# Optimization experiments

Hardware: AMD Instinct MI355X
Metric: run time of the kernel (lower is better)

## Reference

```python
import jax, jax.numpy as jnp
import numpy as np

N_NODES = 50000
N_EDGES = 600000
N_COMM = 500
COMM_EDGES = 8000
NFEAT = 128
NHID = 128
NCLASS = 10
NLAYERS = 3
NHEADS = 8
EPS = 1e-5


def setup_inputs() -> dict:
    key = jax.random.key(0)
    ks = jax.random.split(key, 32)
    s = 0.05
    def rn(i, shape, scale=s):
        return (jax.random.normal(ks[i], shape, dtype=jnp.float32) * scale)
    return {
        "node_features": jax.random.normal(ks[0], (N_NODES, NFEAT), dtype=jnp.float32),
        "node_edge_index": jax.random.randint(ks[1], (2, N_EDGES), 0, N_NODES),
        "comm_features": jax.random.normal(ks[2], (N_COMM, NHID), dtype=jnp.float32),
        "comm_edge_index": jax.random.randint(ks[3], (2, COMM_EDGES), 0, N_COMM),
        "node_to_comm_map": jax.random.randint(ks[4], (N_NODES,), 0, N_COMM),
        # node-branch GCN params (nfeat == nhid so weights stack)
        "node_W": rn(5, (NLAYERS, NHID, NHID)),
        "node_b": rn(6, (NLAYERS, NHID)),
        "node_bn_g": 1.0 + rn(7, (NLAYERS, NHID)),
        "node_bn_b": rn(8, (NLAYERS, NHID)),
        # community-branch GCN params
        "comm_W": rn(9, (NLAYERS, NHID, NHID)),
        "comm_b": rn(10, (NLAYERS, NHID)),
        "comm_bn_g": 1.0 + rn(11, (NLAYERS, NHID)),
        "comm_bn_b": rn(12, (NLAYERS, NHID)),
        # MultiheadAttention params (torch layout: y = x @ W.T + b)
        "attn_in_w": rn(13, (3 * NHID, NHID)),
        "attn_in_b": rn(14, (3 * NHID,)),
        "attn_out_w": rn(15, (NHID, NHID)),
        "attn_out_b": rn(16, (NHID,)),
        # gate LayerNorm
        "ln_g": 1.0 + rn(17, (NHID,)),
        "ln_b": rn(18, (NHID,)),
        # classifier: Linear(128,64) -> BN -> ReLU -> Linear(64,10)
        "cls_W1": rn(19, (NHID, NHID // 2)),
        "cls_b1": rn(20, (NHID // 2,)),
        "cls_bn_g": 1.0 + rn(21, (NHID // 2,)),
        "cls_bn_b": rn(22, (NHID // 2,)),
        "cls_W2": rn(23, (NHID // 2, NCLASS)),
        "cls_b2": rn(24, (NCLASS,)),
    }


def _gcn_norm(edge_index, n):
    # PyG gcn_norm: add self-loops, symmetric D^-1/2 (A+I) D^-1/2
    loop = jnp.arange(n)
    src = jnp.concatenate([edge_index[0], loop])
    dst = jnp.concatenate([edge_index[1], loop])
    deg = jax.ops.segment_sum(jnp.ones(src.shape[0], jnp.float32), dst, num_segments=n)
    dinv = jnp.where(deg > 0, deg ** -0.5, 0.0)
    return src, dst, dinv[src] * dinv[dst]


def _gcn_stack(x, edge_index, Ws, bs, gs, betas):
    n = x.shape[0]
    src, dst, norm = _gcn_norm(edge_index, n)
    h = x
    for i in range(Ws.shape[0]):
        h_prev = h
        m = h @ Ws[i]  # linear commutes with normalized aggregation
        agg = jax.ops.segment_sum(m[src] * norm[:, None], dst, num_segments=n) + bs[i]
        mu = agg.mean(0)
        var = agg.var(0)  # biased, as torch BN training
        hb = (agg - mu) / jnp.sqrt(var + EPS) * gs[i] + betas[i]
        h = jax.nn.relu(hb)
        if i > 0:
            h = h + h_prev
    return h


def _mha(x, wi, bi, wo, bo):
    # x: [N, S=2, E]
    N, S, E = x.shape
    dh = E // NHEADS
    qkv = x @ wi.T + bi
    q, k, v = jnp.split(qkv, 3, axis=-1)
    q = q.reshape(N, S, NHEADS, dh)
    k = k.reshape(N, S, NHEADS, dh)
    v = v.reshape(N, S, NHEADS, dh)
    att = jnp.einsum('nqhd,nkhd->nhqk', q, k) / np.float32(np.sqrt(dh))
    att = jax.nn.softmax(att, axis=-1)
    o = jnp.einsum('nhqk,nkhd->nqhd', att, v).reshape(N, S, E)
    return o @ wo.T + bo


def reference(node_features, node_edge_index, comm_features, comm_edge_index,
              node_to_comm_map, node_W, node_b, node_bn_g, node_bn_b,
              comm_W, comm_b, comm_bn_g, comm_bn_b,
              attn_in_w, attn_in_b, attn_out_w, attn_out_b,
              ln_g, ln_b, cls_W1, cls_b1, cls_bn_g, cls_bn_b, cls_W2, cls_b2):
    h_node = _gcn_stack(node_features, node_edge_index, node_W, node_b, node_bn_g, node_bn_b)
    h_comm = _gcn_stack(comm_features, comm_edge_index, comm_W, comm_b, comm_bn_g, comm_bn_b)
    safe = jnp.clip(node_to_comm_map, 0, h_comm.shape[0] - 1)
    h_comm_exp = h_comm[safe]  # [N, nhid] cross-scale gather
    comb = jnp.stack([h_node, h_comm_exp], axis=1)  # [N, 2, nhid]
    attended = _mha(comb, attn_in_w, attn_in_b, attn_out_w, attn_out_b)
    x = attended.mean(axis=1) + h_node
    mu = x.mean(-1, keepdims=True)
    var = x.var(-1, keepdims=True)
    h_final = (x - mu) / jnp.sqrt(var + EPS) * ln_g + ln_b
    z = h_final @ cls_W1 + cls_b1
    zm = z.mean(0)
    zv = z.var(0)
    z = jax.nn.relu((z - zm) / jnp.sqrt(zv + EPS) * cls_bn_g + cls_bn_b)
    logits = z @ cls_W2 + cls_b2
    return jax.nn.log_softmax(logits, axis=-1)
```

## Files before the change

kernel.cpp:

```cpp
#include <hip/hip_runtime.h>
#include <hip/hip_bf16.h>
#include <cstdint>
#include <cstddef>


typedef __attribute__((ext_vector_type(8))) short bf16x8;
typedef __attribute__((ext_vector_type(4))) float f32x4;

#define EPSV 1e-5f

__device__ __forceinline__ float b2f(unsigned short u) {
    union { unsigned int i; float f; } x; x.i = ((unsigned int)u) << 16; return x.f;
}
__device__ __forceinline__ unsigned short f2b(float f) {
    union { float f; unsigned int i; } x; x.f = f;
    unsigned int i = x.i;
    return (unsigned short)((i + 0x7fffu + ((i >> 16) & 1u)) >> 16);
}

__global__ void prep_kernel(const float* __restrict__ node_W, const float* __restrict__ comm_W,
                            const float* __restrict__ cls_W1, const float* __restrict__ attn_in_w,
                            const float* __restrict__ attn_out_w, const float* __restrict__ comm_feat,
                            const float* __restrict__ node_feat,
                            unsigned short* __restrict__ WtN, unsigned short* __restrict__ WtC,
                            unsigned short* __restrict__ W1t, unsigned short* __restrict__ WinB,
                            unsigned short* __restrict__ WoutB, unsigned short* __restrict__ cfb,
                            unsigned short* __restrict__ nfb, int nC128, int nN128) {
    int idx = blockIdx.x * 256 + threadIdx.x;
    if (idx < 49152) {
        int l = idx >> 14, e = idx & 16383;
        int j = e & 7, lane = (e >> 3) & 63, kc = (e >> 9) & 3, t = e >> 11;
        int col = t * 16 + (lane & 15);
        int k = (lane >> 4) * 8 + kc * 32 + j;
        WtN[idx] = f2b(node_W[l * 16384 + k * 128 + col]); return;
    }
    idx -= 49152;
    if (idx < 49152) {
        int l = idx >> 14, e = idx & 16383;
        int j = e & 7, lane = (e >> 3) & 63, kc = (e >> 9) & 3, t = e >> 11;
        int col = t * 16 + (lane & 15);
        int k = (lane >> 4) * 8 + kc * 32 + j;
        WtC[idx] = f2b(comm_W[l * 16384 + k * 128 + col]); return;
    }
    idx -= 49152;
    if (idx < 8192) {
        int e = idx;
        int j = e & 7, lane = (e >> 3) & 63, kc = (e >> 9) & 3, t = e >> 11;
        int col = t * 16 + (lane & 15);
        int k = (lane >> 4) * 8 + kc * 32 + j;
        W1t[idx] = f2b(cls_W1[k * 64 + col]); return;
    }
    idx -= 8192;
    if (idx < 49152) {
        int e = idx;
        int j = e & 7, lane = (e >> 3) & 63, kc = (e >> 9) & 3, t = e >> 11;
        int col = t * 16 + (lane & 15);
        int k = (lane >> 4) * 8 + kc * 32 + j;
        WinB[idx] = f2b(attn_in_w[col * 128 + k]); return;
    }
    idx -= 49152;
    if (idx < 16384) {
        int e = idx;
        int j = e & 7, lane = (e >> 3) & 63, kc = (e >> 9) & 3, t = e >> 11;
        int col = t * 16 + (lane & 15);
        int k = (lane >> 4) * 8 + kc * 32 + j;
        WoutB[idx] = f2b(attn_out_w[col * 128 + k]); return;
    }
    idx -= 16384;
    if (idx < nC128) { cfb[idx] = f2b(comm_feat[idx]); return; }
    idx -= nC128;
    if (idx < nN128) { nfb[idx] = f2b(node_feat[idx]); }
}

__global__ void count_dual(const int* __restrict__ nd, int* __restrict__ cnt_n, int nE,
                           const int* __restrict__ cd, int* __restrict__ cnt_c, int cE) {
    int t = blockIdx.x * 256 + threadIdx.x;
    if (t < nE) atomicAdd(&cnt_n[nd[t]], 1);
    else if (t - nE < cE) atomicAdd(&cnt_c[cd[t - nE]], 1);
}

__global__ void dinv_dual(const int* __restrict__ cnt_n, float* __restrict__ di_n, int nN,
                          const int* __restrict__ cnt_c, float* __restrict__ di_c, int nC) {
    int t = blockIdx.x * 256 + threadIdx.x;
    if (t < nN) di_n[t] = rsqrtf((float)cnt_n[t] + 1.0f);
    else if (t - nN < nC) di_c[t - nN] = rsqrtf((float)cnt_c[t - nN] + 1.0f);
}

__global__ void scan_block_dual(const int* __restrict__ cnt_n, int* __restrict__ rs_n,
                                int* __restrict__ bsum_n, int nN, int nbN,
                                const int* __restrict__ cnt_c, int* __restrict__ rs_c,
                                int* __restrict__ bsum_c, int nC) {
    __shared__ int tmp[2048];
    const int* cnt; int* excl; int* bsum; int n, lb;
    if ((int)blockIdx.x < nbN) { cnt = cnt_n; excl = rs_n; bsum = bsum_n; n = nN; lb = blockIdx.x; }
    else { cnt = cnt_c; excl = rs_c; bsum = bsum_c; n = nC; lb = blockIdx.x - nbN; }
    int tid = threadIdx.x;
    int gid = lb * 1024 + tid;
    int v = (gid < n) ? ((cnt[gid] + 7) & ~7) : 0;
    int buf = 0;
    tmp[tid] = v;
    __syncthreads();
    for (int d = 1; d < 1024; d <<= 1) {
        int t = tmp[buf * 1024 + tid];
        int add = (tid >= d) ? tmp[buf * 1024 + tid - d] : 0;
        tmp[(1 - buf) * 1024 + tid] = t + add;
        buf = 1 - buf;
        __syncthreads();
    }
    int inc = tmp[buf * 1024 + tid];
    if (gid < n) excl[gid] = inc - v;
    if (tid == 1023) bsum[lb] = inc;
}

__global__ void scan_sums_dual(int* __restrict__ bsum_n, int nbN,
                               int* __restrict__ bsum_c, int nbC) {
    if (threadIdx.x == 0) {
        int acc = 0;
        for (int i = 0; i < nbN; ++i) { int t = bsum_n[i]; bsum_n[i] = acc; acc += t; }
    } else if (threadIdx.x == 1) {
        int acc = 0;
        for (int i = 0; i < nbC; ++i) { int t = bsum_c[i]; bsum_c[i] = acc; acc += t; }
    }
}

__global__ void scan_add_dual(int* __restrict__ rs_n, const int* __restrict__ bsum_n, int nN,
                              int* __restrict__ rs_c, const int* __restrict__ bsum_c, int nC) {
    int gid = blockIdx.x * 256 + threadIdx.x;
    if (gid < nN) rs_n[gid] += bsum_n[gid >> 10];
    else {
        int g = gid - nN;
        if (g < nC) rs_c[g] += bsum_c[g >> 10];
    }
}

__global__ void fill_dual(const int* __restrict__ ns, const int* __restrict__ ndst,
                          const float* __restrict__ di_n, const int* __restrict__ rs_n,
                          int* __restrict__ cur_n, int* __restrict__ csrc_n,
                          float* __restrict__ cw_n, int nE,
                          const int* __restrict__ cs, const int* __restrict__ cdst,
                          const float* __restrict__ di_c, const int* __restrict__ rs_c,
                          int* __restrict__ cur_c, int* __restrict__ csrc_c,
                          float* __restrict__ cw_c, int cE) {
    int e = blockIdx.x * 256 + threadIdx.x;
    if (e < nE) {
        int s = ns[e], d = ndst[e];
        int pos = atomicAdd(&cur_n[d], 1);
        int slot = rs_n[d] + pos;
        csrc_n[slot] = s;
        cw_n[slot] = di_n[s] * di_n[d];
    } else if (e - nE < cE) {
        int ee = e - nE;
        int s = cs[ee], d = cdst[ee];
        int pos = atomicAdd(&cur_c[d], 1);
        int slot = rs_c[d] + pos;
        csrc_c[slot] = s;
        cw_c[slot] = di_c[s] * di_c[d];
    }
}

__device__ __forceinline__ void gemm_wave_128(const unsigned short* __restrict__ A,
                                              const unsigned short* __restrict__ Bt,
                                              unsigned short* __restrict__ D,
                                              int M, int m0, int lane) {
    int r = lane & 15, q = lane >> 4;
    int arow = m0 + r; if (arow >= M) arow = M - 1;
    const unsigned short* ap = A + (size_t)arow * 128 + q * 8;
    bf16x8 afrag[4];
#pragma unroll
    for (int kc = 0; kc < 4; ++kc)
        afrag[kc] = *(const bf16x8*)(const void*)(ap + kc * 32);
#pragma unroll
    for (int tt = 0; tt < 8; ++tt) {
        f32x4 acc = {0.f, 0.f, 0.f, 0.f};
#pragma unroll
        for (int kc = 0; kc < 4; ++kc) {
            bf16x8 bfrag = *(const bf16x8*)(const void*)(Bt + (((size_t)tt * 4 + kc) << 9) + lane * 8);
            acc = __builtin_amdgcn_mfma_f32_16x16x32_bf16(afrag[kc], bfrag, acc, 0, 0, 0);
        }
        int n0 = tt * 16;
#pragma unroll
        for (int t = 0; t < 4; ++t) {
            int row = m0 + q * 4 + t;
            if (row < M) D[(size_t)row * 128 + n0 + r] = f2b(acc[t]);
        }
    }
}

__global__ __launch_bounds__(256) void gemm_dual(
    const unsigned short* __restrict__ A0, const unsigned short* __restrict__ Bt0,
    unsigned short* __restrict__ D0, int M0, int blocksA,
    const unsigned short* __restrict__ A1, const unsigned short* __restrict__ Bt1,
    unsigned short* __restrict__ D1, int M1) {
    int blk = blockIdx.x;
    const unsigned short *A, *Bt; unsigned short* D; int M, lb;
    if (blk < blocksA) { A = A0; Bt = Bt0; D = D0; M = M0; lb = blk; }
    else { A = A1; Bt = Bt1; D = D1; M = M1; lb = blk - blocksA; }
    int m0 = (lb * 4 + (int)(threadIdx.x >> 6)) * 16;
    if (m0 >= M) return;
    gemm_wave_128(A, Bt, D, M, m0, threadIdx.x & 63);
}

__global__ void gemm_kernel(const unsigned short* __restrict__ A,
                            const unsigned short* __restrict__ Bt,
                            const float* __restrict__ bias,
                            float* __restrict__ D, int M, int Ncol) {
    int wave = (blockIdx.x * blockDim.x + threadIdx.x) >> 6;
    int lane = threadIdx.x & 63;
    int m0 = wave * 16;
    if (m0 >= M) return;
    int r = lane & 15, q = lane >> 4;
    int arow = m0 + r; if (arow >= M) arow = M - 1;
    const unsigned short* ap = A + (size_t)arow * 128 + q * 8;
    bf16x8 afrag[4];
#pragma unroll
    for (int kc = 0; kc < 4; ++kc)
        afrag[kc] = *(const bf16x8*)(const void*)(ap + kc * 32);
    int ntiles = Ncol >> 4;
    for (int tt = 0; tt < ntiles; ++tt) {
        f32x4 acc = {0.f, 0.f, 0.f, 0.f};
#pragma unroll
        for (int kc = 0; kc < 4; ++kc) {
            bf16x8 bfrag = *(const bf16x8*)(const void*)(Bt + (((size_t)tt * 4 + kc) << 9) + lane * 8);
            acc = __builtin_amdgcn_mfma_f32_16x16x32_bf16(afrag[kc], bfrag, acc, 0, 0, 0);
        }
        int n0 = tt * 16;
        float bv = bias[n0 + r];
#pragma unroll
        for (int t = 0; t < 4; ++t) {
            int row = m0 + q * 4 + t;
            if (row < M) D[(size_t)row * Ncol + n0 + r] = acc[t] + bv;
        }
    }
}

__global__ __launch_bounds__(256) void gather_dual(
    const unsigned short* __restrict__ m0, const int* __restrict__ rs0,
    const int* __restrict__ cnt0,
    const int* __restrict__ cs0, const float* __restrict__ cw0,
    const float* __restrict__ di0, const float* __restrict__ b0,
    float* __restrict__ agg0, int n0, int blocksA,
    const unsigned short* __restrict__ m1, const int* __restrict__ rs1,
    const int* __restrict__ cnt1,
    const int* __restrict__ cs1, const float* __restrict__ cw1,
    const float* __restrict__ di1, const float* __restrict__ b1,
    float* __restrict__ agg1, int n1) {
    int blk = blockIdx.x;
    const unsigned short* m; const int *rs, *cnt, *cs; const float *cw, *di, *bias;
    float *agg; int n, lb;
    if (blk < blocksA) { m = m0; rs = rs0; cnt = cnt0; cs = cs0; cw = cw0; di = di0; bias = b0; agg = agg0; n = n0; lb = blk; }
    else { m = m1; rs = rs1; cnt = cnt1; cs = cs1; cw = cw1; di = di1; bias = b1; agg = agg1; n = n1; lb = blk - blocksA; }
    int wib = threadIdx.x >> 6, lane = threadIdx.x & 63;
    int node = lb * 4 + wib;
    if (node >= n) return;
    int start = rs[node];
    int end = start + ((cnt[node] + 7) & ~7);
    float a0 = 0.f, a1 = 0.f;
    for (int i = start; i < end; i += 8) {
        int   s[8]; float w[8]; unsigned int v[8];
#pragma unroll
        for (int j = 0; j < 8; ++j) { s[j] = cs[i + j]; w[j] = cw[i + j]; }
#pragma unroll
        for (int j = 0; j < 8; ++j)
            v[j] = *(const unsigned int*)(m + (size_t)s[j] * 128 + 2 * lane);
#pragma unroll
        for (int j = 0; j < 8; ++j) {
            a0 += b2f((unsigned short)(v[j] & 0xffff)) * w[j];
            a1 += b2f((unsigned short)(v[j] >> 16)) * w[j];
        }
    }
    float d = di[node]; float wself = d * d;
    unsigned int v = *(const unsigned int*)(m + (size_t)node * 128 + 2 * lane);
    a0 += b2f((unsigned short)(v & 0xffff)) * wself + bias[2 * lane];
    a1 += b2f((unsigned short)(v >> 16)) * wself + bias[2 * lane + 1];
    float2 o; o.x = a0; o.y = a1;
    ((float2*)(agg + (size_t)node * 128))[lane] = o;
}

__global__ __launch_bounds__(256) void stats_dual(
    const float* __restrict__ agg0, float* __restrict__ sums0, int n0, int blocksA,
    const float* __restrict__ agg1, float* __restrict__ sums1, int n1) {
    __shared__ float rsum[256], rsq[256];
    int blk = blockIdx.x;
    const float* agg; float* sums; int n, lb, nb;
    if (blk < blocksA) { agg = agg0; sums = sums0; n = n0; lb = blk; nb = blocksA; }
    else { agg = agg1; sums = sums1; n = n1; lb = blk - blocksA; nb = gridDim.x - blocksA; }
    int rpb = (n + nb - 1) / nb;
    int t = threadIdx.x;
    int f = t & 127, half = t >> 7;
    int r0 = lb * rpb, r1 = r0 + rpb; if (r1 > n) r1 = n;
    float s = 0.f, s2 = 0.f;
    for (int r = r0 + half; r < r1; r += 2) {
        float v = agg[(size_t)r * 128 + f];
        s += v; s2 += v * v;
    }
    rsum[t] = s; rsq[t] = s2;
    __syncthreads();
    if (t < 128) atomicAdd(&sums[t], rsum[t] + rsum[t + 128]);
    else atomicAdd(&sums[128 + f], rsq[f] + rsq[t]);
}

__global__ __launch_bounds__(256) void apply_dual(
    const float* __restrict__ agg0, const float* __restrict__ sums0,
    const float* __restrict__ g0, const float* __restrict__ be0,
    unsigned short* __restrict__ hb0, int n0, int blocksA, int useRes,
    const float* __restrict__ agg1, const float* __restrict__ sums1,
    const float* __restrict__ g1, const float* __restrict__ be1,
    unsigned short* __restrict__ hb1, int n1) {
    __shared__ float sc[128], sh[128];
    int blk = blockIdx.x;
    const float *agg, *sums, *g, *be; unsigned short* hb; int n, lb;
    if (blk < blocksA) { agg = agg0; sums = sums0; g = g0; be = be0; hb = hb0; n = n0; lb = blk; }
    else { agg = agg1; sums = sums1; g = g1; be = be1; hb = hb1; n = n1; lb = blk - blocksA; }
    int t = threadIdx.x;
    if (t < 128) {
        float inv = 1.f / (float)n;
        float mean = sums[t] * inv;
        float var = sums[128 + t] * inv - mean * mean;
        float rstd = rsqrtf(var + EPSV);
        float s = g[t] * rstd;
        sc[t] = s;
        sh[t] = be[t] - mean * s;
    }
    __syncthreads();
    int base = lb * 1024 + t * 4;
    if (base < n * 128) {
        float4 a = *(const float4*)(agg + base);
        ushort4 h = *(const ushort4*)(hb + base);
        int f = base & 127;
        float v0 = fmaxf(a.x * sc[f] + sh[f], 0.f);
        float v1 = fmaxf(a.y * sc[f + 1] + sh[f + 1], 0.f);
        float v2 = fmaxf(a.z * sc[f + 2] + sh[f + 2], 0.f);
        float v3 = fmaxf(a.w * sc[f + 3] + sh[f + 3], 0.f);
        if (useRes) { v0 += b2f(h.x); v1 += b2f(h.y); v2 += b2f(h.z); v3 += b2f(h.w); }
        ushort4 o; o.x = f2b(v0); o.y = f2b(v1); o.z = f2b(v2); o.w = f2b(v3);
        *(ushort4*)(hb + base) = o;
    }
}

__global__ __launch_bounds__(256) void mha_fused_kernel(
    const unsigned short* __restrict__ hbn, const unsigned short* __restrict__ hbc,
    const int* __restrict__ map,
    const unsigned short* __restrict__ WinB, const float* __restrict__ bin,
    const unsigned short* __restrict__ WoutB, const float* __restrict__ bout,
    const float* __restrict__ lng, const float* __restrict__ lnb,
    unsigned short* __restrict__ hfin, int nN, int nC) {
    __shared__ unsigned short obf_s[16 * 144];
    __shared__ float att_s[8 * 132];

    int b = blockIdx.x;
    int hg = threadIdx.x >> 6;
    int lane = threadIdx.x & 63;
    int r = lane & 15, q = lane >> 4;

    int anode = b * 8 + (r >> 1);
    if (anode >= nN) anode = nN - 1;
    const unsigned short* arow;
    if (r & 1) {
        int c = map[anode]; c = c < 0 ? 0 : (c >= nC ? nC - 1 : c);
        arow = hbc + (size_t)c * 128;
    } else {
        arow = hbn + (size_t)anode * 128;
    }
    bf16x8 afrag[4];
#pragma unroll
    for (int kc = 0; kc < 4; ++kc)
        afrag[kc] = *(const bf16x8*)(const void*)(arow + q * 8 + kc * 32);

    f32x4 qa[2], ka[2], va[2];
#pragma unroll
    for (int p = 0; p < 3; ++p) {
#pragma unroll
        for (int c = 0; c < 2; ++c) {
            int tt = p * 8 + hg * 2 + c;
            f32x4 acc = {0.f, 0.f, 0.f, 0.f};
#pragma unroll
            for (int kc = 0; kc < 4; ++kc) {
                bf16x8 bfrag = *(const bf16x8*)(const void*)(WinB + (((size_t)tt * 4 + kc) << 9) + lane * 8);
                acc = __builtin_amdgcn_mfma_f32_16x16x32_bf16(afrag[kc], bfrag, acc, 0, 0, 0);
            }
            float bv = bin[tt * 16 + r];
#pragma unroll
            for (int t = 0; t < 4; ++t) acc[t] += bv;
            if (p == 0) qa[c] = acc; else if (p == 1) ka[c] = acc; else va[c] = acc;
        }
    }

#pragma unroll
    for (int c = 0; c < 2; ++c) {
        float s00 = qa[c][0] * ka[c][0], s01 = qa[c][0] * ka[c][1];
        float s10 = qa[c][1] * ka[c][0], s11 = qa[c][1] * ka[c][1];
        float u00 = qa[c][2] * ka[c][2], u01 = qa[c][2] * ka[c][3];
        float u10 = qa[c][3] * ka[c][2], u11 = qa[c][3] * ka[c][3];
#pragma unroll
        for (int mku = 1; mku <= 8; mku <<= 1) {
            s00 += __shfl_xor(s00, mku); s01 += __shfl_xor(s01, mku);
            s10 += __shfl_xor(s10, mku); s11 += __shfl_xor(s11, mku);
            u00 += __shfl_xor(u00, mku); u01 += __shfl_xor(u01, mku);
            u10 += __shfl_xor(u10, mku); u11 += __shfl_xor(u11, mku);
        }
        s00 *= 0.25f; s01 *= 0.25f; s10 *= 0.25f; s11 *= 0.25f;
        u00 *= 0.25f; u01 *= 0.25f; u10 *= 0.25f; u11 *= 0.25f;
        float m0 = fmaxf(s00, s01), m1 = fmaxf(s10, s11);
        float m2 = fmaxf(u00, u01), m3 = fmaxf(u10, u11);
        float e00 = __expf(s00 - m0), e01 = __expf(s01 - m0);
        float e10 = __expf(s10 - m1), e11 = __expf(s11 - m1);
        float f00 = __expf(u00 - m2), f01 = __expf(u01 - m2);
        float f10 = __expf(u10 - m3), f11 = __expf(u11 - m3);
        float i0 = 1.f / (e00 + e01), i1 = 1.f / (e10 + e11);
        float i2 = 1.f / (f00 + f01), i3 = 1.f / (f10 + f11);
        float o0 = (e00 * va[c][0] + e01 * va[c][1]) * i0;
        float o1 = (e10 * va[c][0] + e11 * va[c][1]) * i1;
        float o2 = (f00 * va[c][2] + f01 * va[c][3]) * i2;
        float o3 = (f10 * va[c][2] + f11 * va[c][3]) * i3;
        int ocol = (hg * 2 + c) * 16 + r;
        obf_s[(q * 4 + 0) * 144 + ocol] = f2b(o0);
        obf_s[(q * 4 + 1) * 144 + ocol] = f2b(o1);
        obf_s[(q * 4 + 2) * 144 + ocol] = f2b(o2);
        obf_s[(q * 4 + 3) * 144 + ocol] = f2b(o3);
    }
    __syncthreads();

    bf16x8 ofrag[4];
#pragma unroll
    for (int kc = 0; kc < 4; ++kc)
        ofrag[kc] = *(const bf16x8*)(const void*)(obf_s + r * 144 + q * 8 + kc * 32);
#pragma unroll
    for (int c = 0; c < 2; ++c) {
        int tt = hg * 2 + c;
        f32x4 acc = {0.f, 0.f, 0.f, 0.f};
#pragma unroll
        for (int kc = 0; kc < 4; ++kc) {
            bf16x8 bfrag = *(const bf16x8*)(const void*)(WoutB + (((size_t)tt * 4 + kc) << 9) + lane * 8);
            acc = __builtin_amdgcn_mfma_f32_16x16x32_bf16(ofrag[kc], bfrag, acc, 0, 0, 0);
        }
        int n0 = tt * 16;
        float bv = bout[n0 + r];
        att_s[(q * 2 + 0) * 132 + n0 + r] = 0.5f * (acc[0] + acc[1]) + bv;
        att_s[(q * 2 + 1) * 132 + n0 + r] = 0.5f * (acc[2] + acc[3]) + bv;
    }
    __syncthreads();

    {
        int nl = threadIdx.x >> 5;
        int j2 = threadIdx.x & 31;
        int gnode = b * 8 + nl; if (gnode >= nN) gnode = nN - 1;
        const unsigned short* hrow = hbn + (size_t)gnode * 128 + j2 * 4;
        float x[4]; float s = 0.f, s2 = 0.f;
#pragma unroll
        for (int i = 0; i < 4; ++i) {
            x[i] = att_s[nl * 132 + j2 * 4 + i] + b2f(hrow[i]);
            s += x[i]; s2 += x[i] * x[i];
        }
        s += __shfl_xor(s, 1);  s2 += __shfl_xor(s2, 1);
        s += __shfl_xor(s, 2);  s2 += __shfl_xor(s2, 2);
        s += __shfl_xor(s, 4);  s2 += __shfl_xor(s2, 4);
        s += __shfl_xor(s, 8);  s2 += __shfl_xor(s2, 8);
        s += __shfl_xor(s, 16); s2 += __shfl_xor(s2, 16);
        float mu = s * (1.f / 128.f);
        float var = s2 * (1.f / 128.f) - mu * mu;
        float rstd = rsqrtf(var + EPSV);
        ushort4 o;
        o.x = f2b((x[0] - mu) * rstd * lng[j2 * 4]     + lnb[j2 * 4]);
        o.y = f2b((x[1] - mu) * rstd * lng[j2 * 4 + 1] + lnb[j2 * 4 + 1]);
        o.z = f2b((x[2] - mu) * rstd * lng[j2 * 4 + 2] + lnb[j2 * 4 + 2]);
        o.w = f2b((x[3] - mu) * rstd * lng[j2 * 4 + 3] + lnb[j2 * 4 + 3]);
        *(ushort4*)(hfin + (size_t)gnode * 128 + j2 * 4) = o;
    }
}

__global__ __launch_bounds__(256) void stats64_kernel(const float* __restrict__ z,
                                                      float* __restrict__ sums, int N) {
    __shared__ float ls[4][64], lsq[4][64];
    int f = threadIdx.x & 63, rg = threadIdx.x >> 6;
    int r0 = blockIdx.x * 64 + rg * 16;
    int r1 = r0 + 16; if (r1 > N) r1 = N;
    float s = 0.f, s2 = 0.f;
    for (int r = r0; r < r1; ++r) {
        float v = z[(size_t)r * 64 + f];
        s += v; s2 += v * v;
    }
    ls[rg][f] = s; lsq[rg][f] = s2;
    __syncthreads();
    int t = threadIdx.x;
    if (t < 64) atomicAdd(&sums[t], ls[0][t] + ls[1][t] + ls[2][t] + ls[3][t]);
    else if (t < 128) { int c = t - 64; atomicAdd(&sums[64 + c], lsq[0][c] + lsq[1][c] + lsq[2][c] + lsq[3][c]); }
}

__global__ __launch_bounds__(256) void final_kernel(const float* __restrict__ z,
                                                    const float* __restrict__ sums,
                                                    const float* __restrict__ g,
                                                    const float* __restrict__ be,
                                                    const float* __restrict__ W2,
                                                    const float* __restrict__ b2v,
                                                    float* __restrict__ out, int nN) {
    int node = blockIdx.x * 4 + (threadIdx.x >> 6);
    int lane = threadIdx.x & 63;
    float inv = 1.f / (float)nN;
    float mean = sums[lane] * inv;
    float var = sums[64 + lane] * inv - mean * mean;
    float sc = g[lane] * rsqrtf(var + EPSV);
    float sh = be[lane] - mean * sc;
    float v = 0.f;
    if (node < nN) v = fmaxf(z[(size_t)node * 64 + lane] * sc + sh, 0.f);
    float p[10];
    const float* wrow = W2 + lane * 10;
#pragma unroll
    for (int c = 0; c < 10; ++c) p[c] = v * wrow[c];
#pragma unroll
    for (int off = 32; off >= 1; off >>= 1) {
#pragma unroll
        for (int c = 0; c < 10; ++c) p[c] += __shfl_xor(p[c], off);
    }
    if (node >= nN) return;
    float l[10], mx = -1e30f;
#pragma unroll
    for (int c = 0; c < 10; ++c) { l[c] = p[c] + b2v[c]; mx = fmaxf(mx, l[c]); }
    float se = 0.f;
#pragma unroll
    for (int c = 0; c < 10; ++c) se += expf(l[c] - mx);
    float lse = mx + logf(se);
    if (lane < 10) out[(size_t)node * 10 + lane] = l[lane] - lse;
}

static inline int cdiv(long a, long b) { return (int)((a + b - 1) / b); }

extern "C" void kernel_launch(void* const* d_in, const int* in_sizes, int n_in,
                              void* d_out, int out_size, void* d_ws, size_t ws_size,
                              hipStream_t stream) {
    const float* node_feat = (const float*)d_in[0];
    const int*   nedge     = (const int*)d_in[1];
    const float* comm_feat = (const float*)d_in[2];
    const int*   cedge     = (const int*)d_in[3];
    const int*   n2c       = (const int*)d_in[4];
    const float* node_W    = (const float*)d_in[5];
    const float* node_b    = (const float*)d_in[6];
    const float* node_g    = (const float*)d_in[7];
    const float* node_beta = (const float*)d_in[8];
    const float* comm_W    = (const float*)d_in[9];
    const float* comm_b    = (const float*)d_in[10];
    const float* comm_g    = (const float*)d_in[11];
    const float* comm_beta = (const float*)d_in[12];
    const float* attn_in_w = (const float*)d_in[13];
    const float* attn_in_b = (const float*)d_in[14];
    const float* attn_out_w= (const float*)d_in[15];
    const float* attn_out_b= (const float*)d_in[16];
    const float* ln_g      = (const float*)d_in[17];
    const float* ln_b      = (const float*)d_in[18];
    const float* cls_W1    = (const float*)d_in[19];
    const float* cls_b1    = (const float*)d_in[20];
    const float* cls_bn_g  = (const float*)d_in[21];
    const float* cls_bn_b  = (const float*)d_in[22];
    const float* cls_W2    = (const float*)d_in[23];
    const float* cls_b2    = (const float*)d_in[24];

    const int nN = in_sizes[0] / 128;
    const int nE = in_sizes[1] / 2;
    const int nC = in_sizes[2] / 128;
    const int cE = in_sizes[3] / 2;
    const int padE_n = nE + 8 * nN;
    const int padE_c = cE + 8 * nC;

    char* ws = (char*)d_ws;
    size_t off = 0;
    auto alloc = [&](size_t bytes) -> char* {
        char* p = ws + off;
        off = (off + bytes + 255) & ~(size_t)255;
        return p;
    };
    size_t zero_begin = off;
    int*   cnt_n  = (int*)alloc((size_t)nN * 4);
    int*   cur_n  = (int*)alloc((size_t)nN * 4);
    int*   cnt_c  = (int*)alloc((size_t)nC * 4);
    int*   cur_c  = (int*)alloc((size_t)nC * 4);
    float* gsums  = (float*)alloc((size_t)6 * 256 * 4);
    float* csums  = (float*)alloc(128 * 4);
    int*   csrc_n = (int*)alloc((size_t)padE_n * 4);
    float* cw_n   = (float*)alloc((size_t)padE_n * 4);
    int*   csrc_c = (int*)alloc((size_t)padE_c * 4);
    float* cw_c   = (float*)alloc((size_t)padE_c * 4);
    size_t zero_bytes = off - zero_begin;
    int*   rs_n   = (int*)alloc((size_t)(nN + 1) * 4);
    int*   bsum_n = (int*)alloc(256 * 4);
    float* dinv_n = (float*)alloc((size_t)nN * 4);
    int*   rs_c   = (int*)alloc((size_t)(nC + 1) * 4);
    int*   bsum_c = (int*)alloc(256 * 4);
    float* dinv_c = (float*)alloc((size_t)nC * 4);
    unsigned short* hb_n  = (unsigned short*)alloc((size_t)nN * 256);
    unsigned short* hb_c  = (unsigned short*)alloc((size_t)nC * 256);
    unsigned short* cfb   = (unsigned short*)alloc((size_t)nC * 256);
    unsigned short* m_cb  = (unsigned short*)alloc((size_t)nC * 256);
    float*          agg_c = (float*)alloc((size_t)nC * 512);
    unsigned short* WtN  = (unsigned short*)alloc((size_t)3 * 16384 * 2);
    unsigned short* WtC  = (unsigned short*)alloc((size_t)3 * 16384 * 2);
    unsigned short* W1t  = (unsigned short*)alloc((size_t)64 * 128 * 2);
    unsigned short* WinB = (unsigned short*)alloc((size_t)384 * 128 * 2);
    unsigned short* WoutB= (unsigned short*)alloc((size_t)128 * 128 * 2);
    unsigned short* m_nb = (unsigned short*)alloc((size_t)nN * 256);
    float*          agg_n= (float*)alloc((size_t)nN * 512);
    unsigned short* nfb  = (unsigned short*)agg_n;
    unsigned short* hfin = m_nb;
    float*          z    = agg_n;

    hipMemsetAsync(ws + zero_begin, 0, zero_bytes, stream);

    long prepN = 49152L * 3 + 8192 + 16384 + (long)nC * 128 + (long)nN * 128;
    prep_kernel<<<cdiv(prepN, 256), 256, 0, stream>>>(
        node_W, comm_W, cls_W1, attn_in_w, attn_out_w, comm_feat, node_feat,
        WtN, WtC, W1t, WinB, WoutB, cfb, nfb, nC * 128, nN * 128);

    count_dual<<<cdiv((long)nE + cE, 256), 256, 0, stream>>>(nedge + nE, cnt_n, nE, cedge + cE, cnt_c, cE);
    dinv_dual<<<cdiv((long)nN + nC, 256), 256, 0, stream>>>(cnt_n, dinv_n, nN, cnt_c, dinv_c, nC);
    int nbN = cdiv(nN, 1024), nbC = cdiv(nC, 1024);
    scan_block_dual<<<nbN + nbC, 1024, 0, stream>>>(cnt_n, rs_n, bsum_n, nN, nbN, cnt_c, rs_c, bsum_c, nC);
    scan_sums_dual<<<1, 64, 0, stream>>>(bsum_n, nbN, bsum_c, nbC);
    scan_add_dual<<<cdiv((long)nN + nC, 256), 256, 0, stream>>>(rs_n, bsum_n, nN, rs_c, bsum_c, nC);
    fill_dual<<<cdiv((long)nE + cE, 256), 256, 0, stream>>>(
        nedge, nedge + nE, dinv_n, rs_n, cur_n, csrc_n, cw_n, nE,
        cedge, cedge + cE, dinv_c, rs_c, cur_c, csrc_c, cw_c, cE);

    int gemmA = cdiv(nN, 64), gemmB = cdiv(nC, 64);
    int gatA = cdiv(nN, 4), gatB = cdiv(nC, 4);
    int appA = cdiv((long)nN * 128, 1024), appB = cdiv((long)nC * 128, 1024);
    for (int i = 0; i < 3; ++i) {
        const unsigned short* A0 = i == 0 ? nfb : hb_n;
        const unsigned short* A1 = i == 0 ? cfb : hb_c;
        float* s0 = gsums + (size_t)(i * 2 + 0) * 256;
        float* s1 = gsums + (size_t)(i * 2 + 1) * 256;
        gemm_dual<<<gemmA + gemmB, 256, 0, stream>>>(
            A0, WtN + i * 16384, m_nb, nN, gemmA,
            A1, WtC + i * 16384, m_cb, nC);
        gather_dual<<<gatA + gatB, 256, 0, stream>>>(
            m_nb, rs_n, cnt_n, csrc_n, cw_n, dinv_n, node_b + i * 128, agg_n, nN, gatA,
            m_cb, rs_c, cnt_c, csrc_c, cw_c, dinv_c, comm_b + i * 128, agg_c, nC);
        stats_dual<<<256 + 4, 256, 0, stream>>>(agg_n, s0, nN, 256, agg_c, s1, nC);
        apply_dual<<<appA + appB, 256, 0, stream>>>(
            agg_n, s0, node_g + i * 128, node_beta + i * 128, hb_n, nN, appA, i > 0 ? 1 : 0,
            agg_c, s1, comm_g + i * 128, comm_beta + i * 128, hb_c, nC);
    }

    mha_fused_kernel<<<cdiv(nN, 8), 256, 0, stream>>>(
        hb_n, hb_c, n2c, WinB, attn_in_b, WoutB, attn_out_b, ln_g, ln_b, hfin, nN, nC);

    int waves1 = (nN + 15) / 16;
    gemm_kernel<<<cdiv((long)waves1 * 64, 256), 256, 0, stream>>>(
        hfin, W1t, cls_b1, z, nN, 64);
    stats64_kernel<<<cdiv(nN, 64), 256, 0, stream>>>(z, csums, nN);
    final_kernel<<<cdiv(nN, 4), 256, 0, stream>>>(z, csums, cls_bn_g, cls_bn_b,
                                                  cls_W2, cls_b2, (float*)d_out, nN);
}
```

Before: 543.7 us.

## Partition gather feature columns across XCDs for L2 locality

Restructures the SpMM gather so each block handles 16 nodes with 16 lanes each. Blocks are mapped by blockIdx modulo 8 so that each pair of XCDs handles one 32-column feature slice. This is meant to make each XCD's L2 cache only hold a quarter of the message matrix, improving the hit rate for the random neighbor reads. Edge index, weight loads and output stores are made nontemporal to avoid polluting the cache. The trade-off is that each node's edge list is now re-read by four blocks, and the per-lane loads are narrower.

```diff
diff --git a/kernel.cpp b/kernel.cpp
--- a/kernel.cpp
+++ b/kernel.cpp
@@ -249,19 +249,27 @@
     float *agg; int n, lb;
     if (blk < blocksA) { m = m0; rs = rs0; cnt = cnt0; cs = cs0; cw = cw0; di = di0; bias = b0; agg = agg0; n = n0; lb = blk; }
     else { m = m1; rs = rs1; cnt = cnt1; cs = cs1; cw = cw1; di = di1; bias = b1; agg = agg1; n = n1; lb = blk - blocksA; }
-    int wib = threadIdx.x >> 6, lane = threadIdx.x & 63;
-    int node = lb * 4 + wib;
+    int xcd = lb & 7;
+    int slice = xcd >> 1;
+    int group16 = (lb >> 3) * 2 + (xcd & 1);
+    int node = group16 * 16 + (threadIdx.x >> 4);
+    int lane16 = threadIdx.x & 15;
     if (node >= n) return;
     int start = rs[node];
     int end = start + ((cnt[node] + 7) & ~7);
+    int fbase = slice * 32 + 2 * lane16;
+    const unsigned short* mrow = m + fbase;
     float a0 = 0.f, a1 = 0.f;
     for (int i = start; i < end; i += 8) {
-        int   s[8]; float w[8]; unsigned int v[8];
-#pragma unroll
-        for (int j = 0; j < 8; ++j) { s[j] = cs[i + j]; w[j] = cw[i + j]; }
+        int s[8]; float w[8]; unsigned int v[8];
+#pragma unroll
+        for (int j = 0; j < 8; ++j) {
+            s[j] = __builtin_nontemporal_load(cs + i + j);
+            w[j] = __builtin_nontemporal_load(cw + i + j);
+        }
 #pragma unroll
         for (int j = 0; j < 8; ++j)
-            v[j] = *(const unsigned int*)(m + (size_t)s[j] * 128 + 2 * lane);
+            v[j] = *(const unsigned int*)(mrow + (size_t)s[j] * 128);
 #pragma unroll
         for (int j = 0; j < 8; ++j) {
             a0 += b2f((unsigned short)(v[j] & 0xffff)) * w[j];
@@ -269,11 +277,12 @@
         }
     }
     float d = di[node]; float wself = d * d;
-    unsigned int v = *(const unsigned int*)(m + (size_t)node * 128 + 2 * lane);
-    a0 += b2f((unsigned short)(v & 0xffff)) * wself + bias[2 * lane];
-    a1 += b2f((unsigned short)(v >> 16)) * wself + bias[2 * lane + 1];
-    float2 o; o.x = a0; o.y = a1;
-    ((float2*)(agg + (size_t)node * 128))[lane] = o;
+    unsigned int v = *(const unsigned int*)(mrow + (size_t)node * 128);
+    a0 += b2f((unsigned short)(v & 0xffff)) * wself + bias[fbase];
+    a1 += b2f((unsigned short)(v >> 16)) * wself + bias[fbase + 1];
+    union { float2 f2; double d64; } u;
+    u.f2.x = a0; u.f2.y = a1;
+    __builtin_nontemporal_store(u.d64, (double*)(agg + (size_t)node * 128 + fbase));
 }
 
 __global__ __launch_bounds__(256) void stats_dual(
@@ -619,7 +628,8 @@
         cedge, cedge + cE, dinv_c, rs_c, cur_c, csrc_c, cw_c, cE);
 
     int gemmA = cdiv(nN, 64), gemmB = cdiv(nC, 64);
-    int gatA = cdiv(nN, 4), gatB = cdiv(nC, 4);
+    int gatA = cdiv(cdiv(nN, 16), 2) * 8;
+    int gatB = cdiv(cdiv(nC, 16), 2) * 8;
     int appA = cdiv((long)nN * 128, 1024), appB = cdiv((long)nC * 128, 1024);
     for (int i = 0; i < 3; ++i) {
         const unsigned short* A0 = i == 0 ? nfb : hb_n;
```

Measured after the change: 651.0 us. 1.2x slower.

## Pack CSR edge src/weight into int2 and split gather across half-waves

Applied to the files above, without the earlier changes.

Edge source indices and normalized weights are interleaved into a single int2 array, so one load fetches both. The gather kernel now has each half-wave process a different edge, with every lane loading 8 bytes (4 bf16 features), and the halves are combined with a cross-lane shuffle. This halves the per-lane index/weight loads and widens the feature loads, at the cost of a shuffle reduction and idle half-wave lanes in the epilogue.

```diff
diff --git a/kernel.cpp b/kernel.cpp
--- a/kernel.cpp
+++ b/kernel.cpp
@@ -135,26 +135,24 @@
 
 __global__ void fill_dual(const int* __restrict__ ns, const int* __restrict__ ndst,
                           const float* __restrict__ di_n, const int* __restrict__ rs_n,
-                          int* __restrict__ cur_n, int* __restrict__ csrc_n,
-                          float* __restrict__ cw_n, int nE,
+                          int* __restrict__ cur_n, int2* __restrict__ ew_n, int nE,
                           const int* __restrict__ cs, const int* __restrict__ cdst,
                           const float* __restrict__ di_c, const int* __restrict__ rs_c,
-                          int* __restrict__ cur_c, int* __restrict__ csrc_c,
-                          float* __restrict__ cw_c, int cE) {
+                          int* __restrict__ cur_c, int2* __restrict__ ew_c, int cE) {
     int e = blockIdx.x * 256 + threadIdx.x;
     if (e < nE) {
         int s = ns[e], d = ndst[e];
         int pos = atomicAdd(&cur_n[d], 1);
         int slot = rs_n[d] + pos;
-        csrc_n[slot] = s;
-        cw_n[slot] = di_n[s] * di_n[d];
+        int2 p; p.x = s; p.y = __float_as_int(di_n[s] * di_n[d]);
+        ew_n[slot] = p;
     } else if (e - nE < cE) {
         int ee = e - nE;
         int s = cs[ee], d = cdst[ee];
         int pos = atomicAdd(&cur_c[d], 1);
         int slot = rs_c[d] + pos;
-        csrc_c[slot] = s;
-        cw_c[slot] = di_c[s] * di_c[d];
+        int2 p; p.x = s; p.y = __float_as_int(di_c[s] * di_c[d]);
+        ew_c[slot] = p;
     }
 }
 
@@ -235,45 +233,54 @@
 
 __global__ __launch_bounds__(256) void gather_dual(
     const unsigned short* __restrict__ m0, const int* __restrict__ rs0,
-    const int* __restrict__ cnt0,
-    const int* __restrict__ cs0, const float* __restrict__ cw0,
+    const int* __restrict__ cnt0, const int2* __restrict__ ew0,
     const float* __restrict__ di0, const float* __restrict__ b0,
     float* __restrict__ agg0, int n0, int blocksA,
     const unsigned short* __restrict__ m1, const int* __restrict__ rs1,
-    const int* __restrict__ cnt1,
-    const int* __restrict__ cs1, const float* __restrict__ cw1,
+    const int* __restrict__ cnt1, const int2* __restrict__ ew1,
     const float* __restrict__ di1, const float* __restrict__ b1,
     float* __restrict__ agg1, int n1) {
     int blk = blockIdx.x;
-    const unsigned short* m; const int *rs, *cnt, *cs; const float *cw, *di, *bias;
-    float *agg; int n, lb;
-    if (blk < blocksA) { m = m0; rs = rs0; cnt = cnt0; cs = cs0; cw = cw0; di = di0; bias = b0; agg = agg0; n = n0; lb = blk; }
-    else { m = m1; rs = rs1; cnt = cnt1; cs = cs1; cw = cw1; di = di1; bias = b1; agg = agg1; n = n1; lb = blk - blocksA; }
+    const unsigned short* m; const int *rs, *cnt; const int2* ew;
+    const float *di, *bias; float *agg; int n, lb;
+    if (blk < blocksA) { m = m0; rs = rs0; cnt = cnt0; ew = ew0; di = di0; bias = b0; agg = agg0; n = n0; lb = blk; }
+    else { m = m1; rs = rs1; cnt = cnt1; ew = ew1; di = di1; bias = b1; agg = agg1; n = n1; lb = blk - blocksA; }
     int wib = threadIdx.x >> 6, lane = threadIdx.x & 63;
     int node = lb * 4 + wib;
     if (node >= n) return;
     int start = rs[node];
     int end = start + ((cnt[node] + 7) & ~7);
-    float a0 = 0.f, a1 = 0.f;
+    int epair = lane >> 5, hl = lane & 31;
+    const unsigned short* mcol = m + 4 * hl;
+    float a0 = 0.f, a1 = 0.f, a2 = 0.f, a3 = 0.f;
     for (int i = start; i < end; i += 8) {
-        int   s[8]; float w[8]; unsigned int v[8];
-#pragma unroll
-        for (int j = 0; j < 8; ++j) { s[j] = cs[i + j]; w[j] = cw[i + j]; }
-#pragma unroll
-        for (int j = 0; j < 8; ++j)
-            v[j] = *(const unsigned int*)(m + (size_t)s[j] * 128 + 2 * lane);
-#pragma unroll
-        for (int j = 0; j < 8; ++j) {
-            a0 += b2f((unsigned short)(v[j] & 0xffff)) * w[j];
-            a1 += b2f((unsigned short)(v[j] >> 16)) * w[j];
-        }
-    }
-    float d = di[node]; float wself = d * d;
-    unsigned int v = *(const unsigned int*)(m + (size_t)node * 128 + 2 * lane);
-    a0 += b2f((unsigned short)(v & 0xffff)) * wself + bias[2 * lane];
-    a1 += b2f((unsigned short)(v >> 16)) * wself + bias[2 * lane + 1];
-    float2 o; o.x = a0; o.y = a1;
-    ((float2*)(agg + (size_t)node * 128))[lane] = o;
+        int2 e[4]; uint2 v[4];
+#pragma unroll
+        for (int j = 0; j < 4; ++j) e[j] = ew[i + 2 * j + epair];
+#pragma unroll
+        for (int j = 0; j < 4; ++j)
+            v[j] = *(const uint2*)(mcol + (size_t)e[j].x * 128);
+#pragma unroll
+        for (int j = 0; j < 4; ++j) {
+            float w = __int_as_float(e[j].y);
+            a0 += b2f((unsigned short)(v[j].x & 0xffff)) * w;
+            a1 += b2f((unsigned short)(v[j].x >> 16)) * w;
+            a2 += b2f((unsigned short)(v[j].y & 0xffff)) * w;
+            a3 += b2f((unsigned short)(v[j].y >> 16)) * w;
+        }
+    }
+    a0 += __shfl_xor(a0, 32); a1 += __shfl_xor(a1, 32);
+    a2 += __shfl_xor(a2, 32); a3 += __shfl_xor(a3, 32);
+    if (epair == 0) {
+        float d = di[node]; float wself = d * d;
+        uint2 v = *(const uint2*)(mcol + (size_t)node * 128);
+        a0 += b2f((unsigned short)(v.x & 0xffff)) * wself + bias[4 * hl];
+        a1 += b2f((unsigned short)(v.x >> 16)) * wself + bias[4 * hl + 1];
+        a2 += b2f((unsigned short)(v.y & 0xffff)) * wself + bias[4 * hl + 2];
+        a3 += b2f((unsigned short)(v.y >> 16)) * wself + bias[4 * hl + 3];
+        float4 o; o.x = a0; o.y = a1; o.z = a2; o.w = a3;
+        *(float4*)(agg + (size_t)node * 128 + 4 * hl) = o;
+    }
 }
 
 __global__ __launch_bounds__(256) void stats_dual(
@@ -574,10 +581,8 @@
     int*   cur_c  = (int*)alloc((size_t)nC * 4);
     float* gsums  = (float*)alloc((size_t)6 * 256 * 4);
     float* csums  = (float*)alloc(128 * 4);
-    int*   csrc_n = (int*)alloc((size_t)padE_n * 4);
-    float* cw_n   = (float*)alloc((size_t)padE_n * 4);
-    int*   csrc_c = (int*)alloc((size_t)padE_c * 4);
-    float* cw_c   = (float*)alloc((size_t)padE_c * 4);
+    int2*  ew_n   = (int2*)alloc((size_t)padE_n * 8);
+    int2*  ew_c   = (int2*)alloc((size_t)padE_c * 8);
     size_t zero_bytes = off - zero_begin;
     int*   rs_n   = (int*)alloc((size_t)(nN + 1) * 4);
     int*   bsum_n = (int*)alloc(256 * 4);
@@ -615,8 +620,8 @@
     scan_sums_dual<<<1, 64, 0, stream>>>(bsum_n, nbN, bsum_c, nbC);
     scan_add_dual<<<cdiv((long)nN + nC, 256), 256, 0, stream>>>(rs_n, bsum_n, nN, rs_c, bsum_c, nC);
     fill_dual<<<cdiv((long)nE + cE, 256), 256, 0, stream>>>(
-        nedge, nedge + nE, dinv_n, rs_n, cur_n, csrc_n, cw_n, nE,
-        cedge, cedge + cE, dinv_c, rs_c, cur_c, csrc_c, cw_c, cE);
+        nedge, nedge + nE, dinv_n, rs_n, cur_n, ew_n, nE,
+        cedge, cedge + cE, dinv_c, rs_c, cur_c, ew_c, cE);
 
     int gemmA = cdiv(nN, 64), gemmB = cdiv(nC, 64);
     int gatA = cdiv(nN, 4), gatB = cdiv(nC, 4);
@@ -630,8 +635,8 @@
             A0, WtN + i * 16384, m_nb, nN, gemmA,
             A1, WtC + i * 16384, m_cb, nC);
         gather_dual<<<gatA + gatB, 256, 0, stream>>>(
-            m_nb, rs_n, cnt_n, csrc_n, cw_n, dinv_n, node_b + i * 128, agg_n, nN, gatA,
-            m_cb, rs_c, cnt_c, csrc_c, cw_c, dinv_c, comm_b + i * 128, agg_c, nC);
+            m_nb, rs_n, cnt_n, ew_n, dinv_n, node_b + i * 128, agg_n, nN, gatA,
+            m_cb, rs_c, cnt_c, ew_c, dinv_c, comm_b + i * 128, agg_c, nC);
         stats_dual<<<256 + 4, 256, 0, stream>>>(agg_n, s0, nN, 256, agg_c, s1, nC);
         apply_dual<<<appA + appB, 256, 0, stream>>>(
             agg_n, s0, node_g + i * 128, node_beta + i * 128, hb_n, nN, appA, i > 0 ? 1 : 0,
```

Result: no change. 553.8 us (+1.9%).
